# Kernel optimization log

Measured on AMD Instinct MI355X. Metric: run time of the kernel, lower is better.

## Reference

```python
import jax, jax.numpy as jnp
import numpy as np

NH, NKV, D = 16, 8, 128
HID = 2048
EPS = 1e-6
ROPE_BASE = 10000.0
T = 2048


def setup_inputs() -> dict:
    key = jax.random.key(0)
    k1, k2, k3 = jax.random.split(key, 3)
    return {
        "positions": jnp.arange(T, dtype=jnp.int32),
        "hidden_states": jax.random.normal(k1, (T, HID), dtype=jnp.float32),
        "w_qkv": jax.random.normal(k2, (HID, (NH + 2 * NKV) * D), dtype=jnp.float32) * 0.02,
        "w_o": jax.random.normal(k3, (NH * D, HID), dtype=jnp.float32) * 0.02,
        "q_norm_w": jnp.ones((D,), dtype=jnp.float32),
        "k_norm_w": jnp.ones((D,), dtype=jnp.float32),
    }


def _rmsnorm(x, w):
    # per-head RMSNorm over last dim (head_dim)
    return x * jax.lax.rsqrt(jnp.mean(x * x, axis=-1, keepdims=True) + EPS) * w


def reference(positions, hidden_states, w_qkv, w_o, q_norm_w, k_norm_w):
    t = hidden_states.shape[0]
    scale = D ** -0.5

    # fused QKV projection, then split
    qkv = hidden_states @ w_qkv                       # [T, (NH+2*NKV)*D]
    q, k, v = jnp.split(qkv, [NH * D, (NH + NKV) * D], axis=-1)
    q = q.reshape(t, NH, D)
    k = k.reshape(t, NKV, D)
    v = v.reshape(t, NKV, D)

    # per-head QK RMSNorm (Qwen3)
    q = _rmsnorm(q, q_norm_w)
    k = _rmsnorm(k, k_norm_w)

    # RoPE (neox style: rotate half-split pairs)
    inv_freq = 1.0 / (ROPE_BASE ** (jnp.arange(0, D, 2, dtype=jnp.float32) / D))
    freqs = positions.astype(jnp.float32)[:, None] * inv_freq  # [T, D/2]
    cos = jnp.cos(freqs)[:, None, :]                   # [T, 1, D/2]
    sin = jnp.sin(freqs)[:, None, :]

    def rope(x):
        x1, x2 = jnp.split(x, 2, axis=-1)
        return jnp.concatenate([x1 * cos - x2 * sin, x2 * cos + x1 * sin], axis=-1)

    q = rope(q)
    k = rope(k)

    # GQA: repeat kv heads
    g = NH // NKV
    kr = jnp.repeat(k, g, axis=1)                      # [T, NH, D]
    vr = jnp.repeat(v, g, axis=1)

    # causal attention
    scores = jnp.einsum('thd,shd->hts', q, kr) * scale  # [NH, T, T]
    causal = jnp.tril(jnp.ones((t, t), dtype=bool))
    scores = jnp.where(causal[None], scores, -jnp.inf)
    probs = jax.nn.softmax(scores, axis=-1)
    o = jnp.einsum('hts,shd->thd', probs, vr).reshape(t, NH * D)

    return o @ w_o
```

## Files before the change

### kernel.cpp

```cpp
#include <hip/hip_runtime.h>
#include <math.h>

#define T_TOK 2048
#define HIDDEN 2048
#define NH 16
#define NKV 8
#define DH 128

typedef unsigned short u16;
typedef __attribute__((ext_vector_type(8))) short bf16x8;
typedef __attribute__((ext_vector_type(4))) float f32x4;

__device__ __forceinline__ u16 f2bf(float f) {
  union { float f; unsigned u; } x; x.f = f;
  unsigned r = (x.u + 0x7fffu + ((x.u >> 16) & 1u)) >> 16;
  return (u16)r;
}

__device__ __forceinline__ float bf2f(u16 v) {
  union { unsigned u; float f; } x; x.u = ((unsigned)v) << 16;
  return x.f;
}

__device__ __forceinline__ void gload16(const void* g, void* l) {
  __builtin_amdgcn_global_load_lds((const __attribute__((address_space(1))) void*)g,
                                   (__attribute__((address_space(3))) void*)l,
                                   16, 0, 0);
}

__global__ __launch_bounds__(256) void prepass(const float* __restrict__ hidden,
                                               const float* __restrict__ w_qkv,
                                               const float* __restrict__ w_o,
                                               u16* __restrict__ Xb,
                                               u16* __restrict__ WqkvT,
                                               u16* __restrict__ WoT) {
  __shared__ float tile[64][65];
  const int b = blockIdx.x;
  if (b < 4096) {
    int i = b * 256 + threadIdx.x;
    float4 v = ((const float4*)hidden)[i];
    ushort4 o;
    o.x = f2bf(v.x); o.y = f2bf(v.y); o.z = f2bf(v.z); o.w = f2bf(v.w);
    ((ushort4*)Xb)[i] = o;
    return;
  }
  const float* in; u16* out; int R, Cdim, c0, r0;
  if (b < 6144) {
    int bb = b - 4096;
    in = w_qkv; out = WqkvT; R = 2048; Cdim = 4096;
    c0 = (bb & 63) * 64; r0 = (bb >> 6) * 64;
  } else {
    int bb = b - 6144;
    in = w_o; out = WoT; R = 2048; Cdim = 2048;
    c0 = (bb & 31) * 64; r0 = (bb >> 5) * 64;
  }
  const int tx = threadIdx.x & 63, ty = threadIdx.x >> 6;
#pragma unroll
  for (int i = 0; i < 64; i += 4)
    tile[ty + i][tx] = in[(size_t)(r0 + ty + i) * Cdim + c0 + tx];
  __syncthreads();
#pragma unroll
  for (int i = 0; i < 64; i += 4)
    out[(size_t)(c0 + ty + i) * R + r0 + tx] = f2bf(tile[tx][ty + i]);
}

__global__ __launch_bounds__(256) void add_parts2(const u16* __restrict__ a,
                                                  const u16* __restrict__ b,
                                                  float* __restrict__ o, int n4) {
  int i = blockIdx.x * blockDim.x + threadIdx.x;
  if (i < n4) {
    ushort4 x = ((const ushort4*)a)[i], y = ((const ushort4*)b)[i];
    float4 z;
    z.x = bf2f(x.x) + bf2f(y.x);
    z.y = bf2f(x.y) + bf2f(y.y);
    z.z = bf2f(x.z) + bf2f(y.z);
    z.w = bf2f(x.w) + bf2f(y.w);
    ((float4*)o)[i] = z;
  }
}

__global__ __launch_bounds__(256) void rope_vt(const u16* __restrict__ qkv,
                                               const int* __restrict__ pos,
                                               const float* __restrict__ qw,
                                               const float* __restrict__ kw,
                                               u16* __restrict__ Qg,
                                               u16* __restrict__ Kg,
                                               u16* __restrict__ Vt,
                                               unsigned* __restrict__ counter) {
  __shared__ float tile[64][65];
  const int b = blockIdx.x;
  if (b < 12288) {
    const int wave = threadIdx.x >> 6, j = threadIdx.x & 63;
    const int idx = b * 4 + wave;
    const int t = idx & 2047, slot = idx >> 11;
    const float QSC = 0.088388347648318447f * 1.4426950408889634f;
    const size_t base_i = (size_t)t * 4096 + slot * 128;
    float x1 = bf2f(qkv[base_i + j]);
    float x2 = bf2f(qkv[base_i + j + 64]);
    float ss = x1 * x1 + x2 * x2;
#pragma unroll
    for (int m = 1; m < 64; m <<= 1) ss += __shfl_xor(ss, m);
    float r = rsqrtf(ss * (1.0f / 128.0f) + 1e-6f);
    const bool isq = slot < NH;
    const float* w = isq ? qw : kw;
    float xn1 = x1 * r * w[j], xn2 = x2 * r * w[j + 64];
    float fp = (float)pos[t];
    float inv_freq = exp2f(-(float)j * (13.287712379549449f / 64.0f));
    float ang = fp * inv_freq;
    float sn, cs;
    sincosf(ang, &sn, &cs);
    float o1 = xn1 * cs - xn2 * sn;
    float o2 = xn2 * cs + xn1 * sn;
    if (isq) {
      size_t base = ((size_t)slot * T_TOK + t) * DH;
      Qg[base + j] = f2bf(o1 * QSC); Qg[base + 64 + j] = f2bf(o2 * QSC);
    } else {
      size_t base = ((size_t)(slot - NH) * T_TOK + t) * DH;
      Kg[base + j] = f2bf(o1); Kg[base + 64 + j] = f2bf(o2);
    }
    return;
  }
  if (b == 12288 && threadIdx.x == 0) *counter = 0u;
  const int bb = b - 12288;
  const int h = bb & 7, rest = bb >> 3;
  const int t0 = (rest & 31) * 64, d0 = (rest >> 5) * 64;
  const int tx = threadIdx.x & 63, ty = threadIdx.x >> 6;
#pragma unroll
  for (int i = 0; i < 64; i += 4) {
    size_t gi = (size_t)(t0 + ty + i) * 4096 + (NH + NKV) * DH + h * DH + d0 + tx;
    tile[ty + i][tx] = bf2f(qkv[gi]);
  }
  __syncthreads();
  const int sx = ((tx >> 5) * 2 + ((tx >> 2) & 1)) * 16 + ((tx >> 3) & 3) * 4 + (tx & 3);
#pragma unroll
  for (int i = 0; i < 64; i += 4)
    Vt[((size_t)h * DH + d0 + ty + i) * T_TOK + t0 + tx] = f2bf(tile[sx][ty + i]);
}

__global__ __launch_bounds__(512, 2) void gemm128x256(const u16* __restrict__ A,
                                                      const u16* __restrict__ Bt,
                                                      void* __restrict__ Cout,
                                                      int M, int N, int K,
                                                      int lda, int ldb, int obf16) {
  __shared__ __attribute__((aligned(128))) char lds[98304];

  const int nx = N >> 8, ny = M >> 7;
  const int flat = blockIdx.x;
  const int per = gridDim.x >> 3;
  const int swz = (flat & 7) * per + (flat >> 3);
  const int by = swz % ny;
  const int rest = swz / ny;
  const int bx = rest % nx;
  const int bz = rest / nx;
  const int m0 = by << 7, n0 = bx << 8;
  A += (size_t)bz * K;
  Bt += (size_t)bz * K;

  const int tid = threadIdx.x;
  const int wave = tid >> 6, lane = tid & 63;
  const int l15 = lane & 15, quad = lane >> 4;
  const int wr = wave >> 2, wc = wave & 3;

  size_t aoff;
  {
    int chunk = tid;
    int line = chunk >> 3;
    int ls8 = (chunk & 7) ^ (line & 7);
    int row = line * 2 + (ls8 >> 2);
    int ks = ls8 & 3;
    aoff = (size_t)(m0 + row) * lda + ks * 8;
  }
  size_t boff[2];
#pragma unroll
  for (int c = 0; c < 2; ++c) {
    int chunk = c * 512 + tid;
    int line = chunk >> 3;
    int ls8 = (chunk & 7) ^ (line & 7);
    int row = line * 2 + (ls8 >> 2);
    int ks = ls8 & 3;
    boff[c] = (size_t)(n0 + row) * ldb + ks * 8;
  }

#define STAGE(tt) do {                                                   \
    char* da = lds + ((tt) & 3) * 8192 + wave * 1024;                    \
    char* db = lds + 32768 + ((tt) & 3) * 16384 + wave * 1024;           \
    const int kk = (tt) * 32;                                            \
    gload16(A + aoff + kk, da);                                          \
    gload16(Bt + boff[0] + kk, db);                                      \
    gload16(Bt + boff[1] + kk, db + 8192);                               \
  } while (0)

  const int fragoff = (l15 >> 1) * 128 +
                      (((((l15 & 1) << 2) | quad) ^ ((l15 >> 1) & 7)) << 4);

  const f32x4 zero = {0.f, 0.f, 0.f, 0.f};
  f32x4 acc[4][4];
#pragma unroll
  for (int i = 0; i < 4; ++i)
#pragma unroll
    for (int j = 0; j < 4; ++j) acc[i][j] = zero;

  const int NT = K >> 5;
  STAGE(0); STAGE(1); STAGE(2);
  asm volatile("s_waitcnt vmcnt(6)" ::: "memory");
  __builtin_amdgcn_s_barrier();

  for (int t = 0; t < NT; ++t) {
    const char* As = lds + (t & 3) * 8192 + wr * 4096 + fragoff;
    const char* Bs = lds + 32768 + (t & 3) * 16384 + wc * 4096 + fragoff;
    bf16x8 af[4], bfr[4];
#pragma unroll
    for (int mt = 0; mt < 4; ++mt) af[mt] = *(const bf16x8*)(As + mt * 1024);
#pragma unroll
    for (int nt = 0; nt < 4; ++nt) bfr[nt] = *(const bf16x8*)(Bs + nt * 1024);

    if (t + 3 < NT) STAGE(t + 3);

    __builtin_amdgcn_s_setprio(1);
#pragma unroll
    for (int mt = 0; mt < 4; ++mt)
#pragma unroll
      for (int nt = 0; nt < 4; ++nt)
        acc[mt][nt] = __builtin_amdgcn_mfma_f32_16x16x32_bf16(af[mt], bfr[nt], acc[mt][nt], 0, 0, 0);
    __builtin_amdgcn_s_setprio(0);

    const int rem = NT - 1 - t;
    if (rem >= 3)      asm volatile("s_waitcnt vmcnt(6)" ::: "memory");
    else if (rem == 2) asm volatile("s_waitcnt vmcnt(3)" ::: "memory");
    else if (rem == 1) asm volatile("s_waitcnt vmcnt(0)" ::: "memory");
    if (rem > 0) __builtin_amdgcn_s_barrier();
  }
#undef STAGE

  if (obf16) {
    u16* C = (u16*)Cout + (size_t)bz * M * N;
#pragma unroll
    for (int mt = 0; mt < 4; ++mt)
#pragma unroll
      for (int nt = 0; nt < 4; ++nt)
#pragma unroll
        for (int r = 0; r < 4; ++r)
          C[(size_t)(m0 + wr * 64 + mt * 16 + quad * 4 + r) * N + n0 + wc * 64 + nt * 16 + l15] =
              f2bf(acc[mt][nt][r]);
  } else {
    float* C = (float*)Cout + (size_t)bz * M * N;
#pragma unroll
    for (int mt = 0; mt < 4; ++mt)
#pragma unroll
      for (int nt = 0; nt < 4; ++nt)
#pragma unroll
        for (int r = 0; r < 4; ++r)
          C[(size_t)(m0 + wr * 64 + mt * 16 + quad * 4 + r) * N + n0 + wc * 64 + nt * 16 + l15] =
              acc[mt][nt][r];
  }
}

__global__ __launch_bounds__(256) void attn_kernel(const u16* __restrict__ Qg,
                                                   const u16* __restrict__ Kg,
                                                   const u16* __restrict__ Vtg,
                                                   float* __restrict__ Opart,
                                                   float* __restrict__ Lpart,
                                                   unsigned* __restrict__ counter) {
  __shared__ u16 Klds[2][64 * 128];
  __shared__ u16 Vlds[2][128 * 64];
  __shared__ unsigned item_s;
  const int wave = threadIdx.x >> 6, lane = threadIdx.x & 63;
  const int l15 = lane & 15, quad = lane >> 4;
  const f32x4 zero = {0.f, 0.f, 0.f, 0.f};
  const float4 zero4 = {0.f, 0.f, 0.f, 0.f};

#define STAGEKV(jj, sl) do {                                            \
    u16* Kd = &Klds[sl][0]; u16* Vd = &Vlds[sl][0];                     \
    _Pragma("unroll")                                                   \
    for (int c = 0; c < 4; ++c) {                                       \
      int chunk = wave * 4 + c;                                         \
      int sL = chunk * 64 + lane;                                       \
      { int ss = sL >> 4;                                               \
        int g = (sL & 15) ^ (ss & 15);                                  \
        gload16(Kh + ((size_t)((jj) * 64 + ss)) * DH + g * 8, Kd + chunk * 512); } \
      { int d = sL >> 3;                                                \
        int g = (sL & 7) ^ (d & 7);                                     \
        gload16(Vh + (size_t)d * T_TOK + (jj) * 64 + g * 8, Vd + chunk * 512); } \
    } } while (0)

  for (;;) {
    __syncthreads();
    if (threadIdx.x == 0) item_s = atomicAdd(counter, 1u);
    __syncthreads();
    const unsigned item = item_s;
    if (item >= 1024u) break;
    const int qt = 31 - (int)(item >> 5);
    const int s  = (int)(item >> 4) & 1;
    const int h  = (int)item & 15;
    const int kvh = h >> 1;
    const int slot = (h * 32 + qt) * 2 + s;
    const int j0 = s ? (qt + 2) >> 1 : 0;
    const int j1 = s ? qt + 1 : (qt + 2) >> 1;

    float* Oslot = Opart + (size_t)slot * (64 * 128);

    if (j0 >= j1) {
      for (int t = threadIdx.x; t < 64 * 128 / 4; t += 256) ((float4*)Oslot)[t] = zero4;
      if (threadIdx.x < 64) Lpart[slot * 64 + threadIdx.x] = 0.f;
      continue;
    }

    const u16* Qh = Qg + (size_t)h * T_TOK * DH;
    const u16* Kh = Kg + (size_t)kvh * T_TOK * DH;
    const u16* Vh = Vtg + (size_t)kvh * DH * T_TOK;
    const int qrow0 = qt * 64 + wave * 16;

    bf16x8 qf[4];
#pragma unroll
    for (int ks = 0; ks < 4; ++ks)
      qf[ks] = *(const bf16x8*)(Qh + (size_t)(qrow0 + l15) * DH + ks * 32 + quad * 8);

    f32x4 oacc[8];
#pragma unroll
    for (int i = 0; i < 8; ++i) oacc[i] = zero;
    float l_acc = 0.f;

    STAGEKV(j0, 0);
    asm volatile("s_waitcnt vmcnt(0)" ::: "memory");
    __builtin_amdgcn_s_barrier();

    for (int j = j0; j < j1; ++j) {
      const int sl = (j - j0) & 1;
      const bool more = (j + 1 < j1);
      if (more) STAGEKV(j + 1, sl ^ 1);
      const u16* Kl = &Klds[sl][0];
      const u16* Vl = &Vlds[sl][0];

      f32x4 sacc[4];
#pragma unroll
      for (int nt = 0; nt < 4; ++nt) sacc[nt] = zero;
      __builtin_amdgcn_s_setprio(1);
#pragma unroll
      for (int nt = 0; nt < 4; ++nt) {
        int sr = nt * 16 + l15;
#pragma unroll
        for (int ks = 0; ks < 4; ++ks) {
          bf16x8 kf = *(const bf16x8*)&Kl[sr * 128 + (((ks * 4 + quad) ^ (sr & 15)) * 8)];
          sacc[nt] = __builtin_amdgcn_mfma_f32_16x16x32_bf16(kf, qf[ks], sacc[nt], 0, 0, 0);
        }
      }
      __builtin_amdgcn_s_setprio(0);

      if (j == qt) {
        int q = qrow0 + l15;
#pragma unroll
        for (int nt = 0; nt < 4; ++nt)
#pragma unroll
          for (int r = 0; r < 4; ++r) {
            int k = j * 64 + nt * 16 + quad * 4 + r;
            if (k > q) sacc[nt][r] = -INFINITY;
          }
      }

      union { unsigned d[4]; bf16x8 v; } pa[2];
#pragma unroll
      for (int ks = 0; ks < 2; ++ks)
#pragma unroll
        for (int w = 0; w < 4; ++w) {
          int nt = ks * 2 + (w >> 1), rp = (w & 1) * 2;
          unsigned ulo = __float_as_uint(exp2f(sacc[nt][rp]));
          unsigned uhi = __float_as_uint(exp2f(sacc[nt][rp + 1]));
          l_acc += __uint_as_float(ulo & 0xffff0000u) + __uint_as_float(uhi & 0xffff0000u);
          pa[ks].d[w] = (ulo >> 16) | (uhi & 0xffff0000u);
        }

      __builtin_amdgcn_s_setprio(1);
#pragma unroll
      for (int ot = 0; ot < 8; ++ot) {
        int d = ot * 16 + l15;
#pragma unroll
        for (int ks = 0; ks < 2; ++ks) {
          bf16x8 vf = *(const bf16x8*)&Vl[d * 64 + (((ks * 4 + quad) ^ (d & 7)) * 8)];
          oacc[ot] = __builtin_amdgcn_mfma_f32_16x16x32_bf16(pa[ks].v, vf, oacc[ot], 0, 0, 0);
        }
      }
      __builtin_amdgcn_s_setprio(0);

      if (more) {
        asm volatile("s_waitcnt vmcnt(0)" ::: "memory");
        __builtin_amdgcn_s_barrier();
      }
    }

#pragma unroll
    for (int ot = 0; ot < 8; ++ot)
#pragma unroll
      for (int r = 0; r < 4; ++r)
        Oslot[(wave * 16 + quad * 4 + r) * 128 + ot * 16 + l15] = oacc[ot][r];
    l_acc += __shfl_xor(l_acc, 16);
    l_acc += __shfl_xor(l_acc, 32);
    if (quad == 0)
      Lpart[slot * 64 + wave * 16 + l15] = l_acc;
  }
#undef STAGEKV
}

__global__ __launch_bounds__(256) void attn_merge(const float* __restrict__ Opart,
                                                  const float* __restrict__ Lpart,
                                                  u16* __restrict__ Og) {
  const int b = blockIdx.x;
  const int h = b & 15, qt = b >> 4;
  const int slot0 = (h * 32 + qt) * 2, slot1 = slot0 + 1;
  const float4* O0 = (const float4*)(Opart + (size_t)slot0 * (64 * 128));
  const float4* O1 = (const float4*)(Opart + (size_t)slot1 * (64 * 128));
#pragma unroll
  for (int it = 0; it < 8; ++it) {
    int idx = it * 256 + threadIdx.x;
    int r = idx >> 5, c4 = idx & 31;
    float rl = 1.0f / (Lpart[slot0 * 64 + r] + Lpart[slot1 * 64 + r]);
    float4 a = O0[idx], c = O1[idx];
    int row = qt * 64 + r, col = c4 * 4;
    u16* dst = Og + (size_t)row * (NH * DH) + h * DH + col;
    dst[0] = f2bf((a.x + c.x) * rl);
    dst[1] = f2bf((a.y + c.y) * rl);
    dst[2] = f2bf((a.z + c.z) * rl);
    dst[3] = f2bf((a.w + c.w) * rl);
  }
}

extern "C" void kernel_launch(void* const* d_in, const int* in_sizes, int n_in,
                              void* d_out, int out_size, void* d_ws, size_t ws_size,
                              hipStream_t stream) {
  (void)in_sizes; (void)n_in; (void)out_size; (void)ws_size;
  const int* positions = (const int*)d_in[0];
  const float* hidden  = (const float*)d_in[1];
  const float* w_qkv   = (const float*)d_in[2];
  const float* w_o     = (const float*)d_in[3];
  const float* q_norm  = (const float*)d_in[4];
  const float* k_norm  = (const float*)d_in[5];
  float* out = (float*)d_out;

  char* ws = (char*)d_ws;
  u16*   Xb    = (u16*)(ws);
  u16*   WqkvT = (u16*)(ws + ( 8ull << 20));
  u16*   WoT   = (u16*)(ws + (24ull << 20));
  u16*   P0    = (u16*)(ws + (32ull << 20));
  u16*   Qg    = (u16*)(ws + ( 8ull << 20));
  u16*   Kg    = (u16*)(ws + (16ull << 20));
  u16*   Vt    = (u16*)(ws + (20ull << 20));
  u16*   AttnO = (u16*)(ws + (80ull << 20));
  float* Opart = (float*)(ws + (32ull << 20));
  float* Lpart = (float*)(ws);
  unsigned* ctr = (unsigned*)(ws + (512ull << 10));
  u16*   G2P   = (u16*)(ws + (32ull << 20));

  prepass<<<dim3(7168), 256, 0, stream>>>(hidden, w_qkv, w_o, Xb, WqkvT, WoT);

  gemm128x256<<<dim3(256), 512, 0, stream>>>(
      Xb, WqkvT, P0, T_TOK, 4096, HIDDEN, HIDDEN, HIDDEN, 1);

  rope_vt<<<dim3(12288 + 512), 256, 0, stream>>>(P0, positions,
                                                 q_norm, k_norm, Qg, Kg, Vt, ctr);

  attn_kernel<<<dim3(512), 256, 0, stream>>>(Qg, Kg, Vt, Opart, Lpart, ctr);
  attn_merge<<<dim3(512), 256, 0, stream>>>(Opart, Lpart, AttnO);

  gemm128x256<<<dim3(256), 512, 0, stream>>>(
      AttnO, WoT, G2P, T_TOK, HIDDEN, 1024, NH * DH, NH * DH, 1);
  const int n4 = T_TOK * HIDDEN / 4;
  add_parts2<<<dim3(n4 / 256), 256, 0, stream>>>(
      G2P, G2P + (size_t)T_TOK * HIDDEN, out, n4);
}
```

Before: 240.6 us.

## Use 128-row query tiles with 8 waves and variable KV splits

Attention blocks now run 8 waves over a 128-row query tile, so each staged K/V tile is shared by twice as many query rows and the per-wave staging load is halved. Work items are regrouped: the larger query tiles get their KV range split four ways and the smaller ones two ways, which removes the empty split items and the zero-filling of their partial outputs. The merge kernel now sums a variable number of partials over 128-row tiles. The trade-off is per-wave causal masking for the diagonal blocks and bigger blocks, which could lower occupancy.

Measured after the change: 246.5 us. +2.4%, slower.

```diff
diff --git a/kernel.cpp b/kernel.cpp
--- a/kernel.cpp
+++ b/kernel.cpp
@@ -255,7 +255,7 @@
   }
 }
 
-__global__ __launch_bounds__(256) void attn_kernel(const u16* __restrict__ Qg,
+__global__ __launch_bounds__(512) void attn_kernel(const u16* __restrict__ Qg,
                                                    const u16* __restrict__ Kg,
                                                    const u16* __restrict__ Vtg,
                                                    float* __restrict__ Opart,
@@ -267,13 +267,12 @@
   const int wave = threadIdx.x >> 6, lane = threadIdx.x & 63;
   const int l15 = lane & 15, quad = lane >> 4;
   const f32x4 zero = {0.f, 0.f, 0.f, 0.f};
-  const float4 zero4 = {0.f, 0.f, 0.f, 0.f};
 
 #define STAGEKV(jj, sl) do {                                            \
     u16* Kd = &Klds[sl][0]; u16* Vd = &Vlds[sl][0];                     \
     _Pragma("unroll")                                                   \
-    for (int c = 0; c < 4; ++c) {                                       \
-      int chunk = wave * 4 + c;                                         \
+    for (int c = 0; c < 2; ++c) {                                       \
+      int chunk = wave * 2 + c;                                         \
       int sL = chunk * 64 + lane;                                       \
       { int ss = sL >> 4;                                               \
         int g = (sL & 15) ^ (ss & 15);                                  \
@@ -288,27 +287,25 @@
     if (threadIdx.x == 0) item_s = atomicAdd(counter, 1u);
     __syncthreads();
     const unsigned item = item_s;
-    if (item >= 1024u) break;
-    const int qt = 31 - (int)(item >> 5);
-    const int s  = (int)(item >> 4) & 1;
-    const int h  = (int)item & 15;
+    if (item >= 768u) break;
+    const int h = (int)item & 15;
+    const int qxs = (int)(item >> 4);
+    int qt, s, shf;
+    if (qxs < 32) { qt = 15 - (qxs >> 2); s = qxs & 3; shf = 2; }
+    else { int q2 = qxs - 32; qt = 7 - (q2 >> 1); s = q2 & 1; shf = 1; }
+    const int n = 2 * qt + 2;
+    const int j0 = (n * s) >> shf;
+    const int j1 = (n * (s + 1)) >> shf;
+    const int slot = (int)item;
     const int kvh = h >> 1;
-    const int slot = (h * 32 + qt) * 2 + s;
-    const int j0 = s ? (qt + 2) >> 1 : 0;
-    const int j1 = s ? qt + 1 : (qt + 2) >> 1;
-
-    float* Oslot = Opart + (size_t)slot * (64 * 128);
-
-    if (j0 >= j1) {
-      for (int t = threadIdx.x; t < 64 * 128 / 4; t += 256) ((float4*)Oslot)[t] = zero4;
-      if (threadIdx.x < 64) Lpart[slot * 64 + threadIdx.x] = 0.f;
-      continue;
-    }
+
+    float* Oslot = Opart + (size_t)slot * (128 * 128);
 
     const u16* Qh = Qg + (size_t)h * T_TOK * DH;
     const u16* Kh = Kg + (size_t)kvh * T_TOK * DH;
     const u16* Vh = Vtg + (size_t)kvh * DH * T_TOK;
-    const int qrow0 = qt * 64 + wave * 16;
+    const int qrow0 = qt * 128 + wave * 16;
+    const int jq = qrow0 >> 6;
 
     bf16x8 qf[4];
 #pragma unroll
@@ -346,7 +343,7 @@
       }
       __builtin_amdgcn_s_setprio(0);
 
-      if (j == qt) {
+      if (j >= jq) {
         int q = qrow0 + l15;
 #pragma unroll
         for (int nt = 0; nt < 4; ++nt)
@@ -395,7 +392,7 @@
     l_acc += __shfl_xor(l_acc, 16);
     l_acc += __shfl_xor(l_acc, 32);
     if (quad == 0)
-      Lpart[slot * 64 + wave * 16 + l15] = l_acc;
+      Lpart[slot * 128 + wave * 16 + l15] = l_acc;
   }
 #undef STAGEKV
 }
@@ -405,21 +402,35 @@
                                                   u16* __restrict__ Og) {
   const int b = blockIdx.x;
   const int h = b & 15, qt = b >> 4;
-  const int slot0 = (h * 32 + qt) * 2, slot1 = slot0 + 1;
-  const float4* O0 = (const float4*)(Opart + (size_t)slot0 * (64 * 128));
-  const float4* O1 = (const float4*)(Opart + (size_t)slot1 * (64 * 128));
-#pragma unroll
-  for (int it = 0; it < 8; ++it) {
+  int ns, base_qxs;
+  if (qt >= 8) { ns = 4; base_qxs = (15 - qt) * 4; }
+  else         { ns = 2; base_qxs = 32 + (7 - qt) * 2; }
+  int sl[4];
+#pragma unroll
+  for (int s = 0; s < 4; ++s)
+    sl[s] = (base_qxs + (s < ns ? s : 0)) * 16 + h;
+#pragma unroll
+  for (int it = 0; it < 16; ++it) {
     int idx = it * 256 + threadIdx.x;
     int r = idx >> 5, c4 = idx & 31;
-    float rl = 1.0f / (Lpart[slot0 * 64 + r] + Lpart[slot1 * 64 + r]);
-    float4 a = O0[idx], c = O1[idx];
-    int row = qt * 64 + r, col = c4 * 4;
+    float L = Lpart[sl[0] * 128 + r] + Lpart[sl[1] * 128 + r];
+    float4 a = ((const float4*)(Opart + (size_t)sl[0] * 16384))[idx];
+    float4 c = ((const float4*)(Opart + (size_t)sl[1] * 16384))[idx];
+    float4 acc;
+    acc.x = a.x + c.x; acc.y = a.y + c.y; acc.z = a.z + c.z; acc.w = a.w + c.w;
+    if (ns == 4) {
+      L += Lpart[sl[2] * 128 + r] + Lpart[sl[3] * 128 + r];
+      float4 e = ((const float4*)(Opart + (size_t)sl[2] * 16384))[idx];
+      float4 f = ((const float4*)(Opart + (size_t)sl[3] * 16384))[idx];
+      acc.x += e.x + f.x; acc.y += e.y + f.y; acc.z += e.z + f.z; acc.w += e.w + f.w;
+    }
+    float rl = 1.0f / L;
+    int row = qt * 128 + r, col = c4 * 4;
     u16* dst = Og + (size_t)row * (NH * DH) + h * DH + col;
-    dst[0] = f2bf((a.x + c.x) * rl);
-    dst[1] = f2bf((a.y + c.y) * rl);
-    dst[2] = f2bf((a.z + c.z) * rl);
-    dst[3] = f2bf((a.w + c.w) * rl);
+    dst[0] = f2bf(acc.x * rl);
+    dst[1] = f2bf(acc.y * rl);
+    dst[2] = f2bf(acc.z * rl);
+    dst[3] = f2bf(acc.w * rl);
   }
 }
 
@@ -457,8 +468,8 @@
   rope_vt<<<dim3(12288 + 512), 256, 0, stream>>>(P0, positions,
                                                  q_norm, k_norm, Qg, Kg, Vt, ctr);
 
-  attn_kernel<<<dim3(512), 256, 0, stream>>>(Qg, Kg, Vt, Opart, Lpart, ctr);
-  attn_merge<<<dim3(512), 256, 0, stream>>>(Opart, Lpart, AttnO);
+  attn_kernel<<<dim3(512), 512, 0, stream>>>(Qg, Kg, Vt, Opart, Lpart, ctr);
+  attn_merge<<<dim3(256), 256, 0, stream>>>(Opart, Lpart, AttnO);
 
   gemm128x256<<<dim3(256), 512, 0, stream>>>(
       AttnO, WoT, G2P, T_TOK, HIDDEN, 1024, NH * DH, NH * DH, 1);
```

## Pair complementary query tiles per block and drop split-KV merge pass

Applied to the files above, without the earlier changes.

The attention kernel no longer pulls work items from an atomic counter and splits the KV range into two halves. It now launches 256 blocks of 512 threads, each pairing query tile pr with tile 31-pr of one head so every block carries the same causal work. The two tiles share the K/V tiles staged in LDS, and the output is normalised and written as bf16 directly. This removes the fp32 partial-output round trip, the separate merge kernel and the counter reset. The cost is fewer, larger blocks and some waves sitting idle while the high tile finishes its extra KV iterations.

Result: faster. 235.8 us (-2.0%).

```diff
diff --git a/kernel.cpp b/kernel.cpp
--- a/kernel.cpp
+++ b/kernel.cpp
@@ -85,8 +85,7 @@
                                                const float* __restrict__ kw,
                                                u16* __restrict__ Qg,
                                                u16* __restrict__ Kg,
-                                               u16* __restrict__ Vt,
-                                               unsigned* __restrict__ counter) {
+                                               u16* __restrict__ Vt) {
   __shared__ float tile[64][65];
   const int b = blockIdx.x;
   if (b < 12288) {
@@ -120,7 +119,6 @@
     }
     return;
   }
-  if (b == 12288 && threadIdx.x == 0) *counter = 0u;
   const int bb = b - 12288;
   const int h = bb & 7, rest = bb >> 3;
   const int t0 = (rest & 31) * 64, d0 = (rest >> 5) * 64;
@@ -255,25 +253,34 @@
   }
 }
 
-__global__ __launch_bounds__(256) void attn_kernel(const u16* __restrict__ Qg,
+__global__ __launch_bounds__(512) void attn_kernel(const u16* __restrict__ Qg,
                                                    const u16* __restrict__ Kg,
                                                    const u16* __restrict__ Vtg,
-                                                   float* __restrict__ Opart,
-                                                   float* __restrict__ Lpart,
-                                                   unsigned* __restrict__ counter) {
+                                                   u16* __restrict__ Og) {
   __shared__ u16 Klds[2][64 * 128];
   __shared__ u16 Vlds[2][128 * 64];
-  __shared__ unsigned item_s;
-  const int wave = threadIdx.x >> 6, lane = threadIdx.x & 63;
+  const int tid = threadIdx.x;
+  const int wave = tid >> 6, lane = tid & 63;
   const int l15 = lane & 15, quad = lane >> 4;
+  const int b = blockIdx.x;
+  const int h = b & 15, pr = b >> 4;
+  const int kvh = h >> 1;
+  const int qtLO = pr, qtHI = 31 - pr;
+  const int myqt = (wave < 4) ? qtHI : qtLO;
+  const int w4 = wave & 3;
+  const int jmax = qtHI + 1;
   const f32x4 zero = {0.f, 0.f, 0.f, 0.f};
-  const float4 zero4 = {0.f, 0.f, 0.f, 0.f};
+
+  const u16* Qh = Qg + (size_t)h * T_TOK * DH;
+  const u16* Kh = Kg + (size_t)kvh * T_TOK * DH;
+  const u16* Vh = Vtg + (size_t)kvh * DH * T_TOK;
+  const int qrow0 = myqt * 64 + w4 * 16;
 
 #define STAGEKV(jj, sl) do {                                            \
     u16* Kd = &Klds[sl][0]; u16* Vd = &Vlds[sl][0];                     \
     _Pragma("unroll")                                                   \
-    for (int c = 0; c < 4; ++c) {                                       \
-      int chunk = wave * 4 + c;                                         \
+    for (int c = 0; c < 2; ++c) {                                       \
+      int chunk = wave * 2 + c;                                         \
       int sL = chunk * 64 + lane;                                       \
       { int ss = sL >> 4;                                               \
         int g = (sL & 15) ^ (ss & 15);                                  \
@@ -283,51 +290,25 @@
         gload16(Vh + (size_t)d * T_TOK + (jj) * 64 + g * 8, Vd + chunk * 512); } \
     } } while (0)
 
-  for (;;) {
-    __syncthreads();
-    if (threadIdx.x == 0) item_s = atomicAdd(counter, 1u);
-    __syncthreads();
-    const unsigned item = item_s;
-    if (item >= 1024u) break;
-    const int qt = 31 - (int)(item >> 5);
-    const int s  = (int)(item >> 4) & 1;
-    const int h  = (int)item & 15;
-    const int kvh = h >> 1;
-    const int slot = (h * 32 + qt) * 2 + s;
-    const int j0 = s ? (qt + 2) >> 1 : 0;
-    const int j1 = s ? qt + 1 : (qt + 2) >> 1;
-
-    float* Oslot = Opart + (size_t)slot * (64 * 128);
-
-    if (j0 >= j1) {
-      for (int t = threadIdx.x; t < 64 * 128 / 4; t += 256) ((float4*)Oslot)[t] = zero4;
-      if (threadIdx.x < 64) Lpart[slot * 64 + threadIdx.x] = 0.f;
-      continue;
-    }
-
-    const u16* Qh = Qg + (size_t)h * T_TOK * DH;
-    const u16* Kh = Kg + (size_t)kvh * T_TOK * DH;
-    const u16* Vh = Vtg + (size_t)kvh * DH * T_TOK;
-    const int qrow0 = qt * 64 + wave * 16;
-
-    bf16x8 qf[4];
-#pragma unroll
-    for (int ks = 0; ks < 4; ++ks)
-      qf[ks] = *(const bf16x8*)(Qh + (size_t)(qrow0 + l15) * DH + ks * 32 + quad * 8);
-
-    f32x4 oacc[8];
-#pragma unroll
-    for (int i = 0; i < 8; ++i) oacc[i] = zero;
-    float l_acc = 0.f;
-
-    STAGEKV(j0, 0);
-    asm volatile("s_waitcnt vmcnt(0)" ::: "memory");
-    __builtin_amdgcn_s_barrier();
-
-    for (int j = j0; j < j1; ++j) {
-      const int sl = (j - j0) & 1;
-      const bool more = (j + 1 < j1);
-      if (more) STAGEKV(j + 1, sl ^ 1);
+  bf16x8 qf[4];
+#pragma unroll
+  for (int ks = 0; ks < 4; ++ks)
+    qf[ks] = *(const bf16x8*)(Qh + (size_t)(qrow0 + l15) * DH + ks * 32 + quad * 8);
+
+  f32x4 oacc[8];
+#pragma unroll
+  for (int i = 0; i < 8; ++i) oacc[i] = zero;
+  float l_acc = 0.f;
+
+  STAGEKV(0, 0);
+  asm volatile("s_waitcnt vmcnt(0)" ::: "memory");
+  __builtin_amdgcn_s_barrier();
+
+  for (int j = 0; j < jmax; ++j) {
+    const int sl = j & 1;
+    const bool more = (j + 1 < jmax);
+    if (more) STAGEKV(j + 1, sl ^ 1);
+    if (j <= myqt) {
       const u16* Kl = &Klds[sl][0];
       const u16* Vl = &Vlds[sl][0];
 
@@ -346,7 +327,7 @@
       }
       __builtin_amdgcn_s_setprio(0);
 
-      if (j == qt) {
+      if (j >= myqt) {
         int q = qrow0 + l15;
 #pragma unroll
         for (int nt = 0; nt < 4; ++nt)
@@ -380,47 +361,27 @@
         }
       }
       __builtin_amdgcn_s_setprio(0);
-
-      if (more) {
-        asm volatile("s_waitcnt vmcnt(0)" ::: "memory");
-        __builtin_amdgcn_s_barrier();
-      }
     }
 
-#pragma unroll
-    for (int ot = 0; ot < 8; ++ot)
-#pragma unroll
-      for (int r = 0; r < 4; ++r)
-        Oslot[(wave * 16 + quad * 4 + r) * 128 + ot * 16 + l15] = oacc[ot][r];
-    l_acc += __shfl_xor(l_acc, 16);
-    l_acc += __shfl_xor(l_acc, 32);
-    if (quad == 0)
-      Lpart[slot * 64 + wave * 16 + l15] = l_acc;
-  }
+    if (more) {
+      asm volatile("s_waitcnt vmcnt(0)" ::: "memory");
+      __builtin_amdgcn_s_barrier();
+    }
+  }
+
+  l_acc += __shfl_xor(l_acc, 16);
+  l_acc += __shfl_xor(l_acc, 32);
+  float rl[4];
+#pragma unroll
+  for (int r = 0; r < 4; ++r)
+    rl[r] = 1.0f / __shfl(l_acc, quad * 4 + r);
+#pragma unroll
+  for (int ot = 0; ot < 8; ++ot)
+#pragma unroll
+    for (int r = 0; r < 4; ++r)
+      Og[(size_t)(qrow0 + quad * 4 + r) * (NH * DH) + h * DH + ot * 16 + l15] =
+          f2bf(oacc[ot][r] * rl[r]);
 #undef STAGEKV
-}
-
-__global__ __launch_bounds__(256) void attn_merge(const float* __restrict__ Opart,
-                                                  const float* __restrict__ Lpart,
-                                                  u16* __restrict__ Og) {
-  const int b = blockIdx.x;
-  const int h = b & 15, qt = b >> 4;
-  const int slot0 = (h * 32 + qt) * 2, slot1 = slot0 + 1;
-  const float4* O0 = (const float4*)(Opart + (size_t)slot0 * (64 * 128));
-  const float4* O1 = (const float4*)(Opart + (size_t)slot1 * (64 * 128));
-#pragma unroll
-  for (int it = 0; it < 8; ++it) {
-    int idx = it * 256 + threadIdx.x;
-    int r = idx >> 5, c4 = idx & 31;
-    float rl = 1.0f / (Lpart[slot0 * 64 + r] + Lpart[slot1 * 64 + r]);
-    float4 a = O0[idx], c = O1[idx];
-    int row = qt * 64 + r, col = c4 * 4;
-    u16* dst = Og + (size_t)row * (NH * DH) + h * DH + col;
-    dst[0] = f2bf((a.x + c.x) * rl);
-    dst[1] = f2bf((a.y + c.y) * rl);
-    dst[2] = f2bf((a.z + c.z) * rl);
-    dst[3] = f2bf((a.w + c.w) * rl);
-  }
 }
 
 extern "C" void kernel_launch(void* const* d_in, const int* in_sizes, int n_in,
@@ -443,10 +404,7 @@
   u16*   Qg    = (u16*)(ws + ( 8ull << 20));
   u16*   Kg    = (u16*)(ws + (16ull << 20));
   u16*   Vt    = (u16*)(ws + (20ull << 20));
-  u16*   AttnO = (u16*)(ws + (80ull << 20));
-  float* Opart = (float*)(ws + (32ull << 20));
-  float* Lpart = (float*)(ws);
-  unsigned* ctr = (unsigned*)(ws + (512ull << 10));
+  u16*   AttnO = (u16*)(ws + (48ull << 20));
   u16*   G2P   = (u16*)(ws + (32ull << 20));
 
   prepass<<<dim3(7168), 256, 0, stream>>>(hidden, w_qkv, w_o, Xb, WqkvT, WoT);
@@ -455,10 +413,9 @@
       Xb, WqkvT, P0, T_TOK, 4096, HIDDEN, HIDDEN, HIDDEN, 1);
 
   rope_vt<<<dim3(12288 + 512), 256, 0, stream>>>(P0, positions,
-                                                 q_norm, k_norm, Qg, Kg, Vt, ctr);
-
-  attn_kernel<<<dim3(512), 256, 0, stream>>>(Qg, Kg, Vt, Opart, Lpart, ctr);
-  attn_merge<<<dim3(512), 256, 0, stream>>>(Opart, Lpart, AttnO);
+                                                 q_norm, k_norm, Qg, Kg, Vt);
+
+  attn_kernel<<<dim3(256), 512, 0, stream>>>(Qg, Kg, Vt, AttnO);
 
   gemm128x256<<<dim3(256), 512, 0, stream>>>(
       AttnO, WoT, G2P, T_TOK, HIDDEN, 1024, NH * DH, NH * DH, 1);
```
